# Performance work log

Hardware: AMD Instinct MI355X
Metric: run time of the kernel (lower is better)

## Reference

```python
import jax, jax.numpy as jnp
import numpy as np

B, S, E = 256, 512, 768          # batch, seq_len, embed_dim (= 2*hidden_dim)
MD = 2 * 384 + 1                 # memory feature dim after location column = 769
HOPS, OUT = 3, 3


def setup_inputs() -> dict:
    key = jax.random.key(0)
    ks = jax.random.split(key, 9)
    memory = jax.random.normal(ks[0], (B, S, E), dtype=jnp.float32)
    aspect = jax.random.normal(ks[1], (B, E), dtype=jnp.float32)
    att_w = jax.random.normal(ks[2], (MD + 2 * E,), dtype=jnp.float32) * 0.02
    att_b = jnp.zeros((1,), dtype=jnp.float32)
    gru_w_ih = jax.random.normal(ks[3], (3 * E, MD), dtype=jnp.float32) * 0.02
    gru_w_hh = jax.random.normal(ks[4], (3 * E, E), dtype=jnp.float32) * 0.02
    gru_b_ih = jnp.zeros((3 * E,), dtype=jnp.float32)
    gru_b_hh = jnp.zeros((3 * E,), dtype=jnp.float32)
    dense_w = jax.random.normal(ks[5], (E, OUT), dtype=jnp.float32) * 0.02
    dense_b = jnp.zeros((OUT,), dtype=jnp.float32)
    memory_len = jax.random.randint(ks[6], (B,), S // 2, S + 1, dtype=jnp.int32)
    left_len = jax.random.randint(ks[7], (B,), 0, 64, dtype=jnp.int32)
    aspect_len = jax.random.randint(ks[8], (B,), 1, 8, dtype=jnp.int32)
    return dict(memory=memory, aspect=aspect, att_w=att_w, att_b=att_b,
                gru_w_ih=gru_w_ih, gru_w_hh=gru_w_hh, gru_b_ih=gru_b_ih,
                gru_b_hh=gru_b_hh, dense_w=dense_w, dense_b=dense_b,
                memory_len=memory_len, left_len=left_len, aspect_len=aspect_len,
                hops=HOPS)


def _locationed_memory(memory, memory_len, left_len, aspect_len):
    # Vectorized form of the nested python loop: per-position location-decay
    # weight and signed-offset column u, only for idx < memory_len.
    dt = memory.dtype
    idx = jnp.arange(memory.shape[1], dtype=jnp.int32)[None, :]   # [1,S]
    start = left_len[:, None]
    alen = aspect_len[:, None]
    mlen = memory_len[:, None]
    before = idx < start
    after_off = idx - start - alen + 1
    u = jnp.where(before, idx - start,
                  jnp.where(idx < start + alen, 0, after_off)).astype(dt)
    l = jnp.where(before, start - idx,
                  jnp.where(idx < start + alen, 0, after_off)).astype(dt)
    valid = idx < mlen
    w = jnp.where(valid, 1.0 - l / mlen.astype(dt), 1.0)
    u = jnp.where(valid, u, 0.0)
    mem = memory * w[:, :, None]
    return jnp.concatenate([mem, u[:, :, None]], axis=-1)        # [B,S,MD]


def _gru_cell(x, h, w_ih, w_hh, b_ih, b_hh):
    gi = x @ w_ih.T + b_ih
    gh = h @ w_hh.T + b_hh
    ir, iz, in_ = jnp.split(gi, 3, axis=-1)
    hr, hz, hn = jnp.split(gh, 3, axis=-1)
    r = jax.nn.sigmoid(ir + hr)
    z = jax.nn.sigmoid(iz + hz)
    n = jnp.tanh(in_ + r * hn)
    return (1.0 - z) * n + z * h


def reference(memory, aspect, att_w, att_b, gru_w_ih, gru_w_hh, gru_b_ih,
              gru_b_hh, dense_w, dense_b, memory_len, left_len, aspect_len,
              hops):
    mem = _locationed_memory(memory, memory_len, left_len, aspect_len)
    # att_linear(cat([mem, et, aspect])) split into three small matvecs
    w_mem = att_w[:MD]
    w_et = att_w[MD:MD + E]
    w_asp = att_w[MD + E:]
    g_static = mem @ w_mem + (aspect @ w_asp)[:, None] + att_b[0]  # [B,S]
    et = jnp.zeros_like(aspect)
    for _ in range(hops):
        g = g_static + (et @ w_et)[:, None]                        # [B,S]
        alpha = jax.nn.softmax(g, axis=1)
        i = jnp.einsum('bs,bsd->bd', alpha, mem)                   # [B,MD]
        et = _gru_cell(i, et, gru_w_ih, gru_w_hh, gru_b_ih, gru_b_hh)
    logits = et @ dense_w + dense_b                                # [B,OUT]
    return logits
```

## Files before the change

### kernel.cpp

```cpp
#include <hip/hip_runtime.h>
#include <math.h>

#define Bn 256
#define Sn 512
#define En 768
#define G3n 2304

typedef __attribute__((ext_vector_type(8))) short short8;
typedef __attribute__((ext_vector_type(4))) float f32x4;

__device__ __forceinline__ float sigmoidf_(float x) { return 1.f / (1.f + __expf(-x)); }
__device__ __forceinline__ float tanhf_(float x) {
  float e = __expf(2.f * x);
  return (e - 1.f) / (e + 1.f);
}

__device__ __forceinline__ unsigned short f2bf(float x) {
  unsigned int u = __builtin_bit_cast(unsigned int, x);
  u += 0x7FFFu + ((u >> 16) & 1u);
  return (unsigned short)(u >> 16);
}
__device__ __forceinline__ float bf2f(unsigned short u) {
  unsigned int x = ((unsigned int)u) << 16;
  return __builtin_bit_cast(float, x);
}

__device__ __forceinline__ void loc_uw(int s, int start, int al, int ml, float& u, float& w) {
  float uu;
  if (s < start)            uu = (float)(s - start);
  else if (s < start + al)  uu = 0.f;
  else                      uu = (float)(s - start - al + 1);
  float l = fabsf(uu);
  if (s < ml) { w = 1.f - l / (float)ml; u = uu; }
  else        { w = 1.f; u = 0.f; }
}

__global__ __launch_bounds__(1024) void k_mega(
    const float* __restrict__ mem, const float* __restrict__ att_w,
    const int* __restrict__ mlen, const int* __restrict__ llen, const int* __restrict__ alen,
    const float* __restrict__ w_ih, const float* __restrict__ w_hh,
    float* __restrict__ pacc, float* __restrict__ pm,
    float* __restrict__ pz, float* __restrict__ piu,
    unsigned short* __restrict__ wi_bf, unsigned short* __restrict__ wh_bf) {
  __shared__ float accL[16][En];
  __shared__ float mL[16], zL[16], iuL[16];
  int bc = blockIdx.x;
  int tid = threadIdx.x;

  if (bc >= 512) {
    int cb = bc - 512;
    int mat = cb >= 216;
    int t = (cb - mat * 216) * 1024 + tid;
    int idx = t * 8;
    int r = idx / En, c = idx - r * En;
    const float* src;
    unsigned short* dst;
    if (mat == 0) { src = w_ih + (size_t)r * 769 + c; dst = wi_bf + idx; }
    else          { src = w_hh + (size_t)r * En  + c; dst = wh_bf + idx; }
    unsigned int p[4];
#pragma unroll
    for (int j = 0; j < 4; ++j) {
      unsigned int lo = f2bf(src[2 * j]);
      unsigned int hi = f2bf(src[2 * j + 1]);
      p[j] = lo | (hi << 16);
    }
    *reinterpret_cast<uint4*>(dst) = make_uint4(p[0], p[1], p[2], p[3]);
    return;
  }

  int b = bc >> 1, half = bc & 1;
  int wv = tid >> 6, lane = tid & 63;

  float4 w0 = *reinterpret_cast<const float4*>(att_w + lane * 4);
  float4 w1 = *reinterpret_cast<const float4*>(att_w + 256 + lane * 4);
  float4 w2 = *reinterpret_cast<const float4*>(att_w + 512 + lane * 4);
  float wtail = att_w[En];
  int start = llen[b], al = alen[b], ml = mlen[b];
  int s0row = half * 256 + wv * 16;
  const float* base = mem + ((size_t)b * Sn + s0row) * En;

  float m = -1e30f, z = 0.f, iu = 0.f;
  float4 a0 = {0, 0, 0, 0}, a1 = {0, 0, 0, 0}, a2 = {0, 0, 0, 0};
  float4 v0 = *reinterpret_cast<const float4*>(base + lane * 4);
  float4 v1 = *reinterpret_cast<const float4*>(base + 256 + lane * 4);
  float4 v2 = *reinterpret_cast<const float4*>(base + 512 + lane * 4);

  for (int r = 0; r < 16; ++r) {
    float4 c0 = v0, c1 = v1, c2 = v2;
    if (r < 15) {
      const float* nrow = base + (size_t)(r + 1) * En;
      v0 = *reinterpret_cast<const float4*>(nrow + lane * 4);
      v1 = *reinterpret_cast<const float4*>(nrow + 256 + lane * 4);
      v2 = *reinterpret_cast<const float4*>(nrow + 512 + lane * 4);
    }
    float dot = c0.x * w0.x + c0.y * w0.y + c0.z * w0.z + c0.w * w0.w
              + c1.x * w1.x + c1.y * w1.y + c1.z * w1.z + c1.w * w1.w
              + c2.x * w2.x + c2.y * w2.y + c2.z * w2.z + c2.w * w2.w;
#pragma unroll
    for (int off = 32; off; off >>= 1) dot += __shfl_xor(dot, off);
    int s = s0row + r;
    float u, w;
    loc_uw(s, start, al, ml, u, w);
    float g = w * dot + u * wtail;
    if (g > m) {
      float f = __expf(m - g);
      z *= f; iu *= f;
      a0.x *= f; a0.y *= f; a0.z *= f; a0.w *= f;
      a1.x *= f; a1.y *= f; a1.z *= f; a1.w *= f;
      a2.x *= f; a2.y *= f; a2.z *= f; a2.w *= f;
      m = g;
    }
    float e = __expf(g - m);
    z += e; iu += e * u;
    float sc = e * w;
    a0.x += sc * c0.x; a0.y += sc * c0.y; a0.z += sc * c0.z; a0.w += sc * c0.w;
    a1.x += sc * c1.x; a1.y += sc * c1.y; a1.z += sc * c1.z; a1.w += sc * c1.w;
    a2.x += sc * c2.x; a2.y += sc * c2.y; a2.z += sc * c2.z; a2.w += sc * c2.w;
  }

  *reinterpret_cast<float4*>(&accL[wv][lane * 4])       = a0;
  *reinterpret_cast<float4*>(&accL[wv][256 + lane * 4]) = a1;
  *reinterpret_cast<float4*>(&accL[wv][512 + lane * 4]) = a2;
  if (lane == 0) { mL[wv] = m; zL[wv] = z; iuL[wv] = iu; }
  __syncthreads();

  float M = mL[0];
#pragma unroll
  for (int i = 1; i < 16; ++i) M = fmaxf(M, mL[i]);
  float f[16], Z = 0.f, IU = 0.f;
#pragma unroll
  for (int i = 0; i < 16; ++i) {
    f[i] = __expf(mL[i] - M);
    Z += zL[i] * f[i];
    IU += iuL[i] * f[i];
  }
  if (tid < En) {
    float s = 0.f;
#pragma unroll
    for (int i = 0; i < 16; ++i) s += f[i] * accL[i][tid];
    pacc[(size_t)bc * En + tid] = s;
  }
  if (tid == 0) { pm[bc] = M; pz[bc] = Z; piu[bc] = IU; }
}

__global__ __launch_bounds__(256) void k_comb(
    const float* __restrict__ pacc, const float* __restrict__ pm,
    const float* __restrict__ pz, const float* __restrict__ piu,
    unsigned short* __restrict__ ivec_bf, float* __restrict__ ivtail,
    const float* __restrict__ db, float* __restrict__ out) {
  int b = blockIdx.x, tid = threadIdx.x;
  if (b == 0) {
#pragma unroll
    for (int j = 0; j < 3; ++j) {
      int i = tid + j * 256;
      out[i] = db[i % 3];
    }
  }
  float m0 = pm[2 * b], m1 = pm[2 * b + 1];
  float M = fmaxf(m0, m1);
  float f0 = __expf(m0 - M), f1 = __expf(m1 - M);
  float Z = pz[2 * b] * f0 + pz[2 * b + 1] * f1;
  float inv = 1.f / Z;
#pragma unroll
  for (int j = 0; j < 3; ++j) {
    int d = tid + j * 256;
    float s = f0 * pacc[(size_t)(2 * b) * En + d] + f1 * pacc[(size_t)(2 * b + 1) * En + d];
    ivec_bf[(size_t)b * En + d] = f2bf(s * inv);
  }
  if (tid == 0) ivtail[b] = (piu[2 * b] * f0 + piu[2 * b + 1] * f1) * inv;
}

template <int MODE>
__global__ __launch_bounds__(512) void k_fused(
    const unsigned short* __restrict__ Abf, const unsigned short* __restrict__ Wbf,
    const float* __restrict__ ivtail, const float* __restrict__ w_ih,
    const float* __restrict__ b_ih, const float* __restrict__ b_hh,
    float* __restrict__ gi, unsigned short* __restrict__ et_out_bf,
    const float* __restrict__ dw, const float* __restrict__ db,
    float* __restrict__ out) {
  __shared__ unsigned short As[32][264];
  __shared__ unsigned short Bs[3][32][264];
  __shared__ float red[4][64][17];
  int e0 = blockIdx.x * 32, m0 = blockIdx.y * 32;
  int tid = threadIdx.x;
  int lane = tid & 63, wv = tid >> 6;
  int p = wv & 3, kh = wv >> 2;
  int wm = p >> 1, we = p & 1;
  int l15 = lane & 15, l4 = lane >> 4;

  f32x4 acc[3];
#pragma unroll
  for (int g = 0; g < 3; ++g) { acc[g][0] = 0.f; acc[g][1] = 0.f; acc[g][2] = 0.f; acc[g][3] = 0.f; }

  for (int kb = 0; kb < 3; ++kb) {
    int kbase = kb * 256;
    __syncthreads();
#pragma unroll
    for (int i = 0; i < 2; ++i) {
      int idx = tid + i * 512;
      int row = idx >> 5, ch = idx & 31;
      *reinterpret_cast<uint4*>(&As[row][ch * 8]) =
          *reinterpret_cast<const uint4*>(Abf + (size_t)(m0 + row) * En + kbase + ch * 8);
    }
#pragma unroll
    for (int i = 0; i < 6; ++i) {
      int idx = tid + i * 512;
      int g = idx >> 10, rem = idx & 1023;
      int row = rem >> 5, ch = rem & 31;
      *reinterpret_cast<uint4*>(&Bs[g][row][ch * 8]) =
          *reinterpret_cast<const uint4*>(Wbf + (size_t)(g * En + e0 + row) * En + kbase + ch * 8);
    }
    __syncthreads();
#pragma unroll
    for (int ks = 0; ks < 4; ++ks) {
      int col = kh * 128 + ks * 32 + l4 * 8;
      short8 a = *reinterpret_cast<const short8*>(&As[wm * 16 + l15][col]);
#pragma unroll
      for (int g = 0; g < 3; ++g) {
        short8 bfr = *reinterpret_cast<const short8*>(&Bs[g][we * 16 + l15][col]);
        acc[g] = __builtin_amdgcn_mfma_f32_16x16x32_bf16(a, bfr, acc[g], 0, 0, 0);
      }
    }
  }

  if (kh == 1) {
#pragma unroll
    for (int g = 0; g < 3; ++g)
#pragma unroll
      for (int j = 0; j < 4; ++j) red[p][lane][g * 4 + j] = acc[g][j];
  }
  __syncthreads();
  if (kh == 1) return;
#pragma unroll
  for (int g = 0; g < 3; ++g)
#pragma unroll
    for (int j = 0; j < 4; ++j) acc[g][j] += red[p][lane][g * 4 + j];

  int ecol = e0 + we * 16 + l15;
  int mbase = m0 + wm * 16 + l4 * 4;
  float bhr = b_hh[ecol], bhz = b_hh[En + ecol], bhn = b_hh[2 * En + ecol];
  float vout[4];
  if (MODE == 0) {
    float wn0 = w_ih[(size_t)ecol * 769 + En];
    float wn1 = w_ih[(size_t)(En + ecol) * 769 + En];
    float wn2 = w_ih[(size_t)(2 * En + ecol) * 769 + En];
    float bi0 = b_ih[ecol], bi1 = b_ih[En + ecol], bi2 = b_ih[2 * En + ecol];
#pragma unroll
    for (int j = 0; j < 4; ++j) {
      int m = mbase + j;
      float au = ivtail[m];
      float gr = acc[0][j] + au * wn0 + bi0;
      float gz = acc[1][j] + au * wn1 + bi1;
      float gn = acc[2][j] + au * wn2 + bi2;
      gi[(size_t)m * G3n + ecol]          = gr;
      gi[(size_t)m * G3n + En + ecol]     = gz;
      gi[(size_t)m * G3n + 2 * En + ecol] = gn;
      float r = sigmoidf_(gr + bhr);
      float z = sigmoidf_(gz + bhz);
      float n = tanhf_(gn + r * bhn);
      vout[j] = (1.f - z) * n;
    }
  } else {
#pragma unroll
    for (int j = 0; j < 4; ++j) {
      int m = mbase + j;
      float rr = sigmoidf_(gi[(size_t)m * G3n + ecol] + acc[0][j] + bhr);
      float zz = sigmoidf_(gi[(size_t)m * G3n + En + ecol] + acc[1][j] + bhz);
      float nn = tanhf_(gi[(size_t)m * G3n + 2 * En + ecol] + rr * (acc[2][j] + bhn));
      float h = bf2f(Abf[(size_t)m * En + ecol]);
      vout[j] = (1.f - zz) * nn + zz * h;
    }
  }

  if (MODE != 2) {
#pragma unroll
    for (int j = 0; j < 4; ++j)
      et_out_bf[(size_t)(mbase + j) * En + ecol] = f2bf(vout[j]);
  } else {
    float dw0 = dw[ecol * 3 + 0], dw1 = dw[ecol * 3 + 1], dw2 = dw[ecol * 3 + 2];
    float pp[4][3];
#pragma unroll
    for (int j = 0; j < 4; ++j) {
      pp[j][0] = vout[j] * dw0;
      pp[j][1] = vout[j] * dw1;
      pp[j][2] = vout[j] * dw2;
    }
#pragma unroll
    for (int off = 1; off < 16; off <<= 1)
#pragma unroll
      for (int j = 0; j < 4; ++j) {
        pp[j][0] += __shfl_xor(pp[j][0], off);
        pp[j][1] += __shfl_xor(pp[j][1], off);
        pp[j][2] += __shfl_xor(pp[j][2], off);
      }
    if (l15 == 0) {
#pragma unroll
      for (int j = 0; j < 4; ++j) {
        atomicAdd(&out[(mbase + j) * 3 + 0], pp[j][0]);
        atomicAdd(&out[(mbase + j) * 3 + 1], pp[j][1]);
        atomicAdd(&out[(mbase + j) * 3 + 2], pp[j][2]);
      }
    }
  }
}

extern "C" void kernel_launch(void* const* d_in, const int* in_sizes, int n_in,
                              void* d_out, int out_size, void* d_ws, size_t ws_size,
                              hipStream_t stream) {
  const float* memory   = (const float*)d_in[0];
  const float* att_w    = (const float*)d_in[2];
  const float* gru_w_ih = (const float*)d_in[4];
  const float* gru_w_hh = (const float*)d_in[5];
  const float* gru_b_ih = (const float*)d_in[6];
  const float* gru_b_hh = (const float*)d_in[7];
  const float* dense_w  = (const float*)d_in[8];
  const float* dense_b  = (const float*)d_in[9];
  const int* memory_len = (const int*)d_in[10];
  const int* left_len   = (const int*)d_in[11];
  const int* aspect_len = (const int*)d_in[12];
  float* out = (float*)d_out;

  unsigned short* wi_bf   = (unsigned short*)d_ws;
  unsigned short* wh_bf   = wi_bf + (size_t)G3n * En;
  unsigned short* ivec_bf = wh_bf + (size_t)G3n * En;
  unsigned short* eta_bf  = ivec_bf + (size_t)Bn * En;
  unsigned short* etb_bf  = eta_bf + (size_t)Bn * En;
  float* ivtail = (float*)(etb_bf + (size_t)Bn * En);
  float* pm     = ivtail + Bn;
  float* pz     = pm + 2 * Bn;
  float* piu    = pz + 2 * Bn;
  float* pacc   = piu + 2 * Bn;
  float* gi     = pacc + (size_t)2 * Bn * En;

  k_mega<<<dim3(944), 1024, 0, stream>>>(memory, att_w, memory_len, left_len, aspect_len,
                                         gru_w_ih, gru_w_hh, pacc, pm, pz, piu, wi_bf, wh_bf);
  k_comb<<<dim3(Bn), 256, 0, stream>>>(pacc, pm, pz, piu, ivec_bf, ivtail, dense_b, out);
  k_fused<0><<<dim3(En / 32, Bn / 32), 512, 0, stream>>>(
      ivec_bf, wi_bf, ivtail, gru_w_ih, gru_b_ih, gru_b_hh, gi, eta_bf, nullptr, nullptr, nullptr);
  k_fused<1><<<dim3(En / 32, Bn / 32), 512, 0, stream>>>(
      eta_bf, wh_bf, nullptr, nullptr, nullptr, gru_b_hh, gi, etb_bf, nullptr, nullptr, nullptr);
  k_fused<2><<<dim3(En / 32, Bn / 32), 512, 0, stream>>>(
      etb_bf, wh_bf, nullptr, nullptr, nullptr, gru_b_hh, gi, nullptr, dense_w, nullptr, out);
}
```

Measured before the change: 116.7 us.

## Fuse softmax-combine and three GRU hop kernels into one persistent kernel with group barriers

Merges the combine kernel and the three per-hop GEMM+GRU kernels into one persistent kernel of 192 blocks. Blocks synchronize between hops through per-row-group atomic counters in global memory, and the split-softmax combine is folded into the first hop's A-tile load. This removes three kernel launches and the intermediate ivec round trip. In exchange it relies on all 192 blocks being co-resident, because the spin barriers would deadlock otherwise, and it adds spin-wait overhead.

```diff
diff --git a/kernel.cpp b/kernel.cpp
--- a/kernel.cpp
+++ b/kernel.cpp
@@ -5,6 +5,8 @@
 #define Sn 512
 #define En 768
 #define G3n 2304
+#define TAIL_BLOCKS 192
+#define GRP 24
 
 typedef __attribute__((ext_vector_type(8))) short short8;
 typedef __attribute__((ext_vector_type(4))) float f32x4;
@@ -35,13 +37,27 @@
   else        { w = 1.f; u = 0.f; }
 }
 
+__device__ __forceinline__ void group_barrier(unsigned int* cnt, unsigned int expected) {
+  __syncthreads();
+  if (threadIdx.x == 0) {
+    __threadfence();
+    __hip_atomic_fetch_add(cnt, 1u, __ATOMIC_ACQ_REL, __HIP_MEMORY_SCOPE_AGENT);
+    while (__hip_atomic_load(cnt, __ATOMIC_ACQUIRE, __HIP_MEMORY_SCOPE_AGENT) < expected)
+      __builtin_amdgcn_s_sleep(2);
+    __threadfence();
+  }
+  __syncthreads();
+}
+
 __global__ __launch_bounds__(1024) void k_mega(
     const float* __restrict__ mem, const float* __restrict__ att_w,
     const int* __restrict__ mlen, const int* __restrict__ llen, const int* __restrict__ alen,
     const float* __restrict__ w_ih, const float* __restrict__ w_hh,
     float* __restrict__ pacc, float* __restrict__ pm,
     float* __restrict__ pz, float* __restrict__ piu,
-    unsigned short* __restrict__ wi_bf, unsigned short* __restrict__ wh_bf) {
+    unsigned short* __restrict__ wi_bf, unsigned short* __restrict__ wh_bf,
+    const float* __restrict__ db, float* __restrict__ out,
+    unsigned int* __restrict__ barcnt) {
   __shared__ float accL[16][En];
   __shared__ float mL[16], zL[16], iuL[16];
   int bc = blockIdx.x;
@@ -65,6 +81,10 @@
       p[j] = lo | (hi << 16);
     }
     *reinterpret_cast<uint4*>(dst) = make_uint4(p[0], p[1], p[2], p[3]);
+    if (bc == 512) {
+      if (tid < 768)                 out[tid] = db[tid % 3];
+      else if (tid < 768 + 16)       barcnt[tid - 768] = 0u;
+    }
     return;
   }
 
@@ -143,164 +163,185 @@
   if (tid == 0) { pm[bc] = M; pz[bc] = Z; piu[bc] = IU; }
 }
 
-__global__ __launch_bounds__(256) void k_comb(
+__global__ __launch_bounds__(512) void k_tail(
     const float* __restrict__ pacc, const float* __restrict__ pm,
     const float* __restrict__ pz, const float* __restrict__ piu,
-    unsigned short* __restrict__ ivec_bf, float* __restrict__ ivtail,
-    const float* __restrict__ db, float* __restrict__ out) {
-  int b = blockIdx.x, tid = threadIdx.x;
-  if (b == 0) {
-#pragma unroll
-    for (int j = 0; j < 3; ++j) {
-      int i = tid + j * 256;
-      out[i] = db[i % 3];
-    }
-  }
-  float m0 = pm[2 * b], m1 = pm[2 * b + 1];
-  float M = fmaxf(m0, m1);
-  float f0 = __expf(m0 - M), f1 = __expf(m1 - M);
-  float Z = pz[2 * b] * f0 + pz[2 * b + 1] * f1;
-  float inv = 1.f / Z;
-#pragma unroll
-  for (int j = 0; j < 3; ++j) {
-    int d = tid + j * 256;
-    float s = f0 * pacc[(size_t)(2 * b) * En + d] + f1 * pacc[(size_t)(2 * b + 1) * En + d];
-    ivec_bf[(size_t)b * En + d] = f2bf(s * inv);
-  }
-  if (tid == 0) ivtail[b] = (piu[2 * b] * f0 + piu[2 * b + 1] * f1) * inv;
-}
-
-template <int MODE>
-__global__ __launch_bounds__(512) void k_fused(
-    const unsigned short* __restrict__ Abf, const unsigned short* __restrict__ Wbf,
-    const float* __restrict__ ivtail, const float* __restrict__ w_ih,
-    const float* __restrict__ b_ih, const float* __restrict__ b_hh,
-    float* __restrict__ gi, unsigned short* __restrict__ et_out_bf,
-    const float* __restrict__ dw, const float* __restrict__ db,
-    float* __restrict__ out) {
+    const unsigned short* __restrict__ wi_bf, const unsigned short* __restrict__ wh_bf,
+    const float* __restrict__ w_ih, const float* __restrict__ b_ih,
+    const float* __restrict__ b_hh, float* __restrict__ gi,
+    unsigned short* __restrict__ eta_bf, unsigned short* __restrict__ etb_bf,
+    const float* __restrict__ dw, float* __restrict__ out,
+    unsigned int* __restrict__ barcnt) {
   __shared__ unsigned short As[32][264];
   __shared__ unsigned short Bs[3][32][264];
   __shared__ float red[4][64][17];
-  int e0 = blockIdx.x * 32, m0 = blockIdx.y * 32;
+  __shared__ float rowF0[32], rowF1[32], rowAu[32];
+  int bid = blockIdx.x;
+  int mgrp = bid / GRP;
+  int e0 = (bid - mgrp * GRP) * 32, m0 = mgrp * 32;
   int tid = threadIdx.x;
   int lane = tid & 63, wv = tid >> 6;
   int p = wv & 3, kh = wv >> 2;
   int wm = p >> 1, we = p & 1;
   int l15 = lane & 15, l4 = lane >> 4;
 
-  f32x4 acc[3];
-#pragma unroll
-  for (int g = 0; g < 3; ++g) { acc[g][0] = 0.f; acc[g][1] = 0.f; acc[g][2] = 0.f; acc[g][3] = 0.f; }
-
-  for (int kb = 0; kb < 3; ++kb) {
-    int kbase = kb * 256;
+  if (tid < 32) {
+    int m = m0 + tid;
+    float ma = pm[2 * m], mb = pm[2 * m + 1];
+    float M = fmaxf(ma, mb);
+    float f0 = __expf(ma - M), f1 = __expf(mb - M);
+    float iv = 1.f / (pz[2 * m] * f0 + pz[2 * m + 1] * f1);
+    rowF0[tid] = f0 * iv;
+    rowF1[tid] = f1 * iv;
+    rowAu[tid] = (piu[2 * m] * f0 + piu[2 * m + 1] * f1) * iv;
+  }
+
+  for (int hop = 0; hop < 3; ++hop) {
+    const unsigned short* Wbf = (hop == 0) ? wi_bf : wh_bf;
+    const unsigned short* Abf = (hop == 1) ? eta_bf : etb_bf;
+
+    f32x4 acc[3];
+#pragma unroll
+    for (int g = 0; g < 3; ++g) { acc[g][0] = 0.f; acc[g][1] = 0.f; acc[g][2] = 0.f; acc[g][3] = 0.f; }
+
+    for (int kb = 0; kb < 3; ++kb) {
+      int kbase = kb * 256;
+      __syncthreads();
+      if (hop == 0) {
+#pragma unroll
+        for (int i = 0; i < 2; ++i) {
+          int idx = tid + i * 512;
+          int row = idx >> 5, ch = idx & 31;
+          float f0 = rowF0[row], f1 = rowF1[row];
+          const float* q0 = pacc + (size_t)(2 * (m0 + row)) * En + kbase + ch * 8;
+          const float* q1 = q0 + En;
+          float4 x0 = *reinterpret_cast<const float4*>(q0);
+          float4 x1 = *reinterpret_cast<const float4*>(q0 + 4);
+          float4 y0 = *reinterpret_cast<const float4*>(q1);
+          float4 y1 = *reinterpret_cast<const float4*>(q1 + 4);
+          unsigned int pk[4];
+          pk[0] = (unsigned int)f2bf(f0 * x0.x + f1 * y0.x)
+                | ((unsigned int)f2bf(f0 * x0.y + f1 * y0.y) << 16);
+          pk[1] = (unsigned int)f2bf(f0 * x0.z + f1 * y0.z)
+                | ((unsigned int)f2bf(f0 * x0.w + f1 * y0.w) << 16);
+          pk[2] = (unsigned int)f2bf(f0 * x1.x + f1 * y1.x)
+                | ((unsigned int)f2bf(f0 * x1.y + f1 * y1.y) << 16);
+          pk[3] = (unsigned int)f2bf(f0 * x1.z + f1 * y1.z)
+                | ((unsigned int)f2bf(f0 * x1.w + f1 * y1.w) << 16);
+          *reinterpret_cast<uint4*>(&As[row][ch * 8]) = make_uint4(pk[0], pk[1], pk[2], pk[3]);
+        }
+      } else {
+#pragma unroll
+        for (int i = 0; i < 2; ++i) {
+          int idx = tid + i * 512;
+          int row = idx >> 5, ch = idx & 31;
+          *reinterpret_cast<uint4*>(&As[row][ch * 8]) =
+              *reinterpret_cast<const uint4*>(Abf + (size_t)(m0 + row) * En + kbase + ch * 8);
+        }
+      }
+#pragma unroll
+      for (int i = 0; i < 6; ++i) {
+        int idx = tid + i * 512;
+        int g = idx >> 10, rem = idx & 1023;
+        int row = rem >> 5, ch = rem & 31;
+        *reinterpret_cast<uint4*>(&Bs[g][row][ch * 8]) =
+            *reinterpret_cast<const uint4*>(Wbf + (size_t)(g * En + e0 + row) * En + kbase + ch * 8);
+      }
+      __syncthreads();
+#pragma unroll
+      for (int ks = 0; ks < 4; ++ks) {
+        int col = kh * 128 + ks * 32 + l4 * 8;
+        short8 a = *reinterpret_cast<const short8*>(&As[wm * 16 + l15][col]);
+#pragma unroll
+        for (int g = 0; g < 3; ++g) {
+          short8 bfr = *reinterpret_cast<const short8*>(&Bs[g][we * 16 + l15][col]);
+          acc[g] = __builtin_amdgcn_mfma_f32_16x16x32_bf16(a, bfr, acc[g], 0, 0, 0);
+        }
+      }
+    }
+
     __syncthreads();
-#pragma unroll
-    for (int i = 0; i < 2; ++i) {
-      int idx = tid + i * 512;
-      int row = idx >> 5, ch = idx & 31;
-      *reinterpret_cast<uint4*>(&As[row][ch * 8]) =
-          *reinterpret_cast<const uint4*>(Abf + (size_t)(m0 + row) * En + kbase + ch * 8);
-    }
-#pragma unroll
-    for (int i = 0; i < 6; ++i) {
-      int idx = tid + i * 512;
-      int g = idx >> 10, rem = idx & 1023;
-      int row = rem >> 5, ch = rem & 31;
-      *reinterpret_cast<uint4*>(&Bs[g][row][ch * 8]) =
-          *reinterpret_cast<const uint4*>(Wbf + (size_t)(g * En + e0 + row) * En + kbase + ch * 8);
+    if (kh == 1) {
+#pragma unroll
+      for (int g = 0; g < 3; ++g)
+#pragma unroll
+        for (int j = 0; j < 4; ++j) red[p][lane][g * 4 + j] = acc[g][j];
     }
     __syncthreads();
-#pragma unroll
-    for (int ks = 0; ks < 4; ++ks) {
-      int col = kh * 128 + ks * 32 + l4 * 8;
-      short8 a = *reinterpret_cast<const short8*>(&As[wm * 16 + l15][col]);
-#pragma unroll
-      for (int g = 0; g < 3; ++g) {
-        short8 bfr = *reinterpret_cast<const short8*>(&Bs[g][we * 16 + l15][col]);
-        acc[g] = __builtin_amdgcn_mfma_f32_16x16x32_bf16(a, bfr, acc[g], 0, 0, 0);
+    if (kh == 0) {
+#pragma unroll
+      for (int g = 0; g < 3; ++g)
+#pragma unroll
+        for (int j = 0; j < 4; ++j) acc[g][j] += red[p][lane][g * 4 + j];
+
+      int ecol = e0 + we * 16 + l15;
+      int mbase = m0 + wm * 16 + l4 * 4;
+      float bhr = b_hh[ecol], bhz = b_hh[En + ecol], bhn = b_hh[2 * En + ecol];
+      float vout[4];
+      if (hop == 0) {
+        float wn0 = w_ih[(size_t)ecol * 769 + En];
+        float wn1 = w_ih[(size_t)(En + ecol) * 769 + En];
+        float wn2 = w_ih[(size_t)(2 * En + ecol) * 769 + En];
+        float bi0 = b_ih[ecol], bi1 = b_ih[En + ecol], bi2 = b_ih[2 * En + ecol];
+#pragma unroll
+        for (int j = 0; j < 4; ++j) {
+          int m = mbase + j;
+          float au = rowAu[wm * 16 + l4 * 4 + j];
+          float gr = acc[0][j] + au * wn0 + bi0;
+          float gz = acc[1][j] + au * wn1 + bi1;
+          float gn = acc[2][j] + au * wn2 + bi2;
+          gi[(size_t)m * G3n + ecol]          = gr;
+          gi[(size_t)m * G3n + En + ecol]     = gz;
+          gi[(size_t)m * G3n + 2 * En + ecol] = gn;
+          float r = sigmoidf_(gr + bhr);
+          float z = sigmoidf_(gz + bhz);
+          float n = tanhf_(gn + r * bhn);
+          vout[j] = (1.f - z) * n;
+          eta_bf[(size_t)m * En + ecol] = f2bf(vout[j]);
+        }
+      } else {
+#pragma unroll
+        for (int j = 0; j < 4; ++j) {
+          int m = mbase + j;
+          float rr = sigmoidf_(gi[(size_t)m * G3n + ecol] + acc[0][j] + bhr);
+          float zz = sigmoidf_(gi[(size_t)m * G3n + En + ecol] + acc[1][j] + bhz);
+          float nn = tanhf_(gi[(size_t)m * G3n + 2 * En + ecol] + rr * (acc[2][j] + bhn));
+          float h = bf2f(Abf[(size_t)m * En + ecol]);
+          vout[j] = (1.f - zz) * nn + zz * h;
+        }
+        if (hop == 1) {
+#pragma unroll
+          for (int j = 0; j < 4; ++j)
+            etb_bf[(size_t)(mbase + j) * En + ecol] = f2bf(vout[j]);
+        } else {
+          float dw0 = dw[ecol * 3 + 0], dw1 = dw[ecol * 3 + 1], dw2 = dw[ecol * 3 + 2];
+          float pp[4][3];
+#pragma unroll
+          for (int j = 0; j < 4; ++j) {
+            pp[j][0] = vout[j] * dw0;
+            pp[j][1] = vout[j] * dw1;
+            pp[j][2] = vout[j] * dw2;
+          }
+#pragma unroll
+          for (int off = 1; off < 16; off <<= 1)
+#pragma unroll
+            for (int j = 0; j < 4; ++j) {
+              pp[j][0] += __shfl_xor(pp[j][0], off);
+              pp[j][1] += __shfl_xor(pp[j][1], off);
+              pp[j][2] += __shfl_xor(pp[j][2], off);
+            }
+          if (l15 == 0) {
+#pragma unroll
+            for (int j = 0; j < 4; ++j) {
+              atomicAdd(&out[(mbase + j) * 3 + 0], pp[j][0]);
+              atomicAdd(&out[(mbase + j) * 3 + 1], pp[j][1]);
+              atomicAdd(&out[(mbase + j) * 3 + 2], pp[j][2]);
+            }
+          }
+        }
       }
     }
-  }
-
-  if (kh == 1) {
-#pragma unroll
-    for (int g = 0; g < 3; ++g)
-#pragma unroll
-      for (int j = 0; j < 4; ++j) red[p][lane][g * 4 + j] = acc[g][j];
-  }
-  __syncthreads();
-  if (kh == 1) return;
-#pragma unroll
-  for (int g = 0; g < 3; ++g)
-#pragma unroll
-    for (int j = 0; j < 4; ++j) acc[g][j] += red[p][lane][g * 4 + j];
-
-  int ecol = e0 + we * 16 + l15;
-  int mbase = m0 + wm * 16 + l4 * 4;
-  float bhr = b_hh[ecol], bhz = b_hh[En + ecol], bhn = b_hh[2 * En + ecol];
-  float vout[4];
-  if (MODE == 0) {
-    float wn0 = w_ih[(size_t)ecol * 769 + En];
-    float wn1 = w_ih[(size_t)(En + ecol) * 769 + En];
-    float wn2 = w_ih[(size_t)(2 * En + ecol) * 769 + En];
-    float bi0 = b_ih[ecol], bi1 = b_ih[En + ecol], bi2 = b_ih[2 * En + ecol];
-#pragma unroll
-    for (int j = 0; j < 4; ++j) {
-      int m = mbase + j;
-      float au = ivtail[m];
-      float gr = acc[0][j] + au * wn0 + bi0;
-      float gz = acc[1][j] + au * wn1 + bi1;
-      float gn = acc[2][j] + au * wn2 + bi2;
-      gi[(size_t)m * G3n + ecol]          = gr;
-      gi[(size_t)m * G3n + En + ecol]     = gz;
-      gi[(size_t)m * G3n + 2 * En + ecol] = gn;
-      float r = sigmoidf_(gr + bhr);
-      float z = sigmoidf_(gz + bhz);
-      float n = tanhf_(gn + r * bhn);
-      vout[j] = (1.f - z) * n;
-    }
-  } else {
-#pragma unroll
-    for (int j = 0; j < 4; ++j) {
-      int m = mbase + j;
-      float rr = sigmoidf_(gi[(size_t)m * G3n + ecol] + acc[0][j] + bhr);
-      float zz = sigmoidf_(gi[(size_t)m * G3n + En + ecol] + acc[1][j] + bhz);
-      float nn = tanhf_(gi[(size_t)m * G3n + 2 * En + ecol] + rr * (acc[2][j] + bhn));
-      float h = bf2f(Abf[(size_t)m * En + ecol]);
-      vout[j] = (1.f - zz) * nn + zz * h;
-    }
-  }
-
-  if (MODE != 2) {
-#pragma unroll
-    for (int j = 0; j < 4; ++j)
-      et_out_bf[(size_t)(mbase + j) * En + ecol] = f2bf(vout[j]);
-  } else {
-    float dw0 = dw[ecol * 3 + 0], dw1 = dw[ecol * 3 + 1], dw2 = dw[ecol * 3 + 2];
-    float pp[4][3];
-#pragma unroll
-    for (int j = 0; j < 4; ++j) {
-      pp[j][0] = vout[j] * dw0;
-      pp[j][1] = vout[j] * dw1;
-      pp[j][2] = vout[j] * dw2;
-    }
-#pragma unroll
-    for (int off = 1; off < 16; off <<= 1)
-#pragma unroll
-      for (int j = 0; j < 4; ++j) {
-        pp[j][0] += __shfl_xor(pp[j][0], off);
-        pp[j][1] += __shfl_xor(pp[j][1], off);
-        pp[j][2] += __shfl_xor(pp[j][2], off);
-      }
-    if (l15 == 0) {
-#pragma unroll
-      for (int j = 0; j < 4; ++j) {
-        atomicAdd(&out[(mbase + j) * 3 + 0], pp[j][0]);
-        atomicAdd(&out[(mbase + j) * 3 + 1], pp[j][1]);
-        atomicAdd(&out[(mbase + j) * 3 + 2], pp[j][2]);
-      }
-    }
+    if (hop < 2) group_barrier(&barcnt[hop * 8 + mgrp], GRP);
   }
 }
 
@@ -320,25 +361,21 @@
   const int* aspect_len = (const int*)d_in[12];
   float* out = (float*)d_out;
 
-  unsigned short* wi_bf   = (unsigned short*)d_ws;
-  unsigned short* wh_bf   = wi_bf + (size_t)G3n * En;
-  unsigned short* ivec_bf = wh_bf + (size_t)G3n * En;
-  unsigned short* eta_bf  = ivec_bf + (size_t)Bn * En;
-  unsigned short* etb_bf  = eta_bf + (size_t)Bn * En;
-  float* ivtail = (float*)(etb_bf + (size_t)Bn * En);
-  float* pm     = ivtail + Bn;
+  unsigned short* wi_bf  = (unsigned short*)d_ws;
+  unsigned short* wh_bf  = wi_bf + (size_t)G3n * En;
+  unsigned short* eta_bf = wh_bf + (size_t)G3n * En;
+  unsigned short* etb_bf = eta_bf + (size_t)Bn * En;
+  float* pm     = (float*)(etb_bf + (size_t)Bn * En);
   float* pz     = pm + 2 * Bn;
   float* piu    = pz + 2 * Bn;
   float* pacc   = piu + 2 * Bn;
   float* gi     = pacc + (size_t)2 * Bn * En;
+  unsigned int* barcnt = (unsigned int*)(gi + (size_t)Bn * G3n);
 
   k_mega<<<dim3(944), 1024, 0, stream>>>(memory, att_w, memory_len, left_len, aspect_len,
-                                         gru_w_ih, gru_w_hh, pacc, pm, pz, piu, wi_bf, wh_bf);
-  k_comb<<<dim3(Bn), 256, 0, stream>>>(pacc, pm, pz, piu, ivec_bf, ivtail, dense_b, out);
-  k_fused<0><<<dim3(En / 32, Bn / 32), 512, 0, stream>>>(
-      ivec_bf, wi_bf, ivtail, gru_w_ih, gru_b_ih, gru_b_hh, gi, eta_bf, nullptr, nullptr, nullptr);
-  k_fused<1><<<dim3(En / 32, Bn / 32), 512, 0, stream>>>(
-      eta_bf, wh_bf, nullptr, nullptr, nullptr, gru_b_hh, gi, etb_bf, nullptr, nullptr, nullptr);
-  k_fused<2><<<dim3(En / 32, Bn / 32), 512, 0, stream>>>(
-      etb_bf, wh_bf, nullptr, nullptr, nullptr, gru_b_hh, gi, nullptr, dense_w, nullptr, out);
-}
+                                         gru_w_ih, gru_w_hh, pacc, pm, pz, piu, wi_bf, wh_bf,
+                                         dense_b, out, barcnt);
+  k_tail<<<dim3(TAIL_BLOCKS), 512, 0, stream>>>(pacc, pm, pz, piu, wi_bf, wh_bf,
+                                                gru_w_ih, gru_b_ih, gru_b_hh, gi,
+                                                eta_bf, etb_bf, dense_w, out, barcnt);
+}
```

Result: slower. 138.6 us (+18.8%).
